# Performance work log

Measured on AMD Instinct MI355X. Metric: run time of the kernel, lower is better.

Reference implementation:

```python
import jax, jax.numpy as jnp
import numpy as np

N_EMBD = 512
N_HEAD = 8
D_HEAD = N_EMBD // N_HEAD
N_EXPERTS = 4
TOP_K = 2
D_FF = 4 * N_EMBD
EPS_RMS = 1e-5


def setup_inputs() -> dict:
    key = jax.random.key(0)
    ks = jax.random.split(key, 10)
    B, T, C = 8, 1024, N_EMBD
    s = 0.02
    return {
        "x": jax.random.normal(ks[0], (B, T, C), jnp.float32),
        "ln1_w": jnp.ones((C,), jnp.float32),
        "ln2_w": jnp.ones((C,), jnp.float32),
        "wq": jax.random.normal(ks[1], (C, C), jnp.float32) * s,
        "wk": jax.random.normal(ks[2], (C, C), jnp.float32) * s,
        "wv": jax.random.normal(ks[3], (C, C), jnp.float32) * s,
        "wo": jax.random.normal(ks[4], (C, C), jnp.float32) * s,
        "gate_w": jax.random.normal(ks[5], (N_EXPERTS, C), jnp.float32) * s,
        "w_fc": jax.random.normal(ks[6], (N_EXPERTS, D_FF, C), jnp.float32) * s,
        "w_proj": jax.random.normal(ks[7], (N_EXPERTS, C, D_FF), jnp.float32) * s,
    }


def rms_norm(x, w):
    var = jnp.mean(x * x, axis=-1, keepdims=True)
    return x * jax.lax.rsqrt(var + EPS_RMS) * w


def causal_attention(x, wq, wk, wv, wo):
    B, T, C = x.shape
    q = (x @ wq.T).reshape(B, T, N_HEAD, D_HEAD)
    k = (x @ wk.T).reshape(B, T, N_HEAD, D_HEAD)
    v = (x @ wv.T).reshape(B, T, N_HEAD, D_HEAD)
    scores = jnp.einsum("bqhd,bkhd->bhqk", q, k) / jnp.sqrt(jnp.float32(D_HEAD))
    mask = jnp.tril(jnp.ones((T, T), bool))
    scores = jnp.where(mask, scores, jnp.finfo(scores.dtype).min)
    attn = jax.nn.softmax(scores, axis=-1)
    out = jnp.einsum("bhqk,bkhd->bqhd", attn, v).reshape(B, T, C)
    return out @ wo.T


def ds_moe(x, gate_w, w_fc, w_proj):
    B, T, C = x.shape
    xf = x.reshape(B * T, C)                                # [N, C]
    gate_logits = xf @ gate_w.T                             # [N, E]
    gate_probs = jax.nn.softmax(gate_logits, axis=-1)
    topw, topi = jax.lax.top_k(gate_probs, TOP_K)           # [N, K]
    topw = topw / jnp.clip(topw.sum(-1, keepdims=True), 1e-6)
    # sparse router weights [N, E] (scatter of normalized top-k)
    sparse_w = jnp.zeros((xf.shape[0], N_EXPERTS), xf.dtype)
    sparse_w = sparse_w.at[jnp.arange(xf.shape[0])[:, None], topi].set(topw)
    # dense-equivalent expert compute: out = sum_e w_e * MLP_e(x)
    h = jax.nn.gelu(jnp.einsum("nc,efc->enf", xf, w_fc), approximate=False)
    eo = jnp.einsum("enf,ecf->enc", h, w_proj)              # [E, N, C]
    out = jnp.einsum("ne,enc->nc", sparse_w, eo)
    return out.reshape(B, T, C), sparse_w


def reference(x, ln1_w, ln2_w, wq, wk, wv, wo, gate_w, w_fc, w_proj):
    x = x + causal_attention(rms_norm(x, ln1_w), wq, wk, wv, wo)
    moe_out, router_w = ds_moe(rms_norm(x, ln2_w), gate_w, w_fc, w_proj)
    x = x + moe_out
    return x, router_w
```

## Files before the change

kernel.cpp:

```cpp
#include <hip/hip_runtime.h>
#include <math.h>

typedef __bf16 bf16_t;
typedef float    f32x2 __attribute__((ext_vector_type(2)));
typedef float    f32x4 __attribute__((ext_vector_type(4)));
typedef unsigned u32x2 __attribute__((ext_vector_type(2)));
typedef unsigned u32x4 __attribute__((ext_vector_type(4)));
typedef __bf16   bf16x8 __attribute__((ext_vector_type(8)));

#define WS_MB (size_t)(1u << 20)

__device__ __forceinline__ void gl16(const bf16_t* g, bf16_t* l) {
    void* gnc = const_cast<void*>((const void*)g);
    __builtin_amdgcn_global_load_lds((__attribute__((address_space(1))) void*)gnc,
                                     (__attribute__((address_space(3))) void*)l,
                                     16, 0, 0);
}

__device__ __forceinline__ float dot4(f32x4 a, f32x4 b) {
    return a.x * b.x + a.y * b.y + a.z * b.z + a.w * b.w;
}

__device__ __forceinline__ int xcd_swz(int orig, int nwg) {
    int q = nwg >> 3, r = nwg & 7;
    int x = orig & 7, i = orig >> 3;
    int base = (x < r) ? x * (q + 1) : r * (q + 1) + (x - r) * q;
    return base + i;
}

__global__ __launch_bounds__(256) void cvt_all_kernel(
    const float* __restrict__ s0, const float* __restrict__ s1,
    const float* __restrict__ s2, const float* __restrict__ s3,
    const float* __restrict__ s4, const float* __restrict__ s5,
    bf16_t* __restrict__ d0, bf16_t* __restrict__ d1,
    bf16_t* __restrict__ d2, bf16_t* __restrict__ d3,
    bf16_t* __restrict__ d4, bf16_t* __restrict__ d5,
    int* __restrict__ cnt) {
    if (blockIdx.x == 0 && threadIdx.x < 4) cnt[threadIdx.x] = 0;
    int i = blockIdx.x * 256 + threadIdx.x;
    const float* s; bf16_t* d; int off;
    if (i < 262144) {
        int seg = i >> 16; off = i & 65535;
        s = seg == 0 ? s0 : seg == 1 ? s1 : seg == 2 ? s2 : s3;
        d = seg == 0 ? d0 : seg == 1 ? d1 : seg == 2 ? d2 : d3;
    } else if (i < 1310720) { s = s4; d = d4; off = i - 262144; }
    else                    { s = s5; d = d5; off = i - 1310720; }
    f32x4 v = ((const f32x4*)s)[off];
    union { bf16_t b[4]; u32x2 u; } p;
    p.b[0] = (bf16_t)v.x; p.b[1] = (bf16_t)v.y;
    p.b[2] = (bf16_t)v.z; p.b[3] = (bf16_t)v.w;
    ((u32x2*)d)[off] = p.u;
}

__global__ __launch_bounds__(256) void rmsnorm_kernel(const float* __restrict__ x,
                                                      const float* __restrict__ w,
                                                      bf16_t* __restrict__ out) {
    int row = blockIdx.x;
    const float* xr = x + (size_t)row * 512;
    int t = threadIdx.x;
    f32x2 v = *(const f32x2*)(xr + t * 2);
    float ss = v.x * v.x + v.y * v.y;
#pragma unroll
    for (int o = 32; o > 0; o >>= 1) ss += __shfl_down(ss, o);
    __shared__ float red[4];
    if ((t & 63) == 0) red[t >> 6] = ss;
    __syncthreads();
    float tot = (red[0] + red[1]) + (red[2] + red[3]);
    float sc = rsqrtf(tot * (1.0f / 512.0f) + 1e-5f);
    f32x2 wv = *(const f32x2*)(w + t * 2);
    union { bf16_t b[2]; unsigned u; } p;
    p.b[0] = (bf16_t)(v.x * sc * wv.x);
    p.b[1] = (bf16_t)(v.y * sc * wv.y);
    *(unsigned*)(out + (size_t)row * 512 + t * 2) = p.u;
}

__device__ inline float gelu_fast(float x) {
    float u = -1.5957691216f * x * fmaf(0.044715f * x, x, 1.0f);
    return x / (1.0f + __expf(u));
}

#define GEMM_COMPUTE(LA, LB)                                                          \
    _Pragma("unroll")                                                                 \
    for (int kk = 0; kk < 2; ++kk) {                                                  \
        bf16x8 af[4], bfr[4];                                                         \
        _Pragma("unroll")                                                             \
        for (int mi = 0; mi < 4; mi++)                                                \
            af[mi] = *(const bf16x8*)((LA) + (wr + mi * 16 + lrow) * 64               \
                                      + (((kk * 4 + sg) ^ lr3) * 8));                 \
        _Pragma("unroll")                                                             \
        for (int ni = 0; ni < 4; ni++)                                                \
            bfr[ni] = *(const bf16x8*)((LB) + (wc + ni * 16 + lrow) * 64              \
                                       + (((kk * 4 + sg) ^ lr3) * 8));                \
        _Pragma("unroll")                                                             \
        for (int mi = 0; mi < 4; mi++) {                                              \
            _Pragma("unroll")                                                         \
            for (int ni = 0; ni < 4; ni++) {                                          \
                acc[mi][ni] = __builtin_amdgcn_mfma_f32_16x16x32_bf16(                \
                    af[mi], bfr[ni], acc[mi][ni], 0, 0, 0);                           \
            }                                                                         \
        }                                                                             \
    }

template <int EPI>
__global__ __launch_bounds__(256) void gemm_kernel(const bf16_t* __restrict__ A,
                                                   const bf16_t* __restrict__ B,
                                                   void* __restrict__ C,
                                                   const float* __restrict__ aux,
                                                   int N, int K, int ncol) {
    const int id = xcd_swz(blockIdx.x, gridDim.x);
    const int row0 = (id / ncol) * 128;
    const int col0 = (id % ncol) * 128;
    __shared__ __align__(16) bf16_t lds_a[128 * 64];
    __shared__ __align__(16) bf16_t lds_b[128 * 64];
    const int t = threadIdx.x;
    const bf16_t* Ap = A + (size_t)row0 * K;
    const bf16_t* Bp = B + (size_t)col0 * K;
    const int lane = t & 63, wave = t >> 6;
    const int wr = (wave >> 1) * 64, wc = (wave & 1) * 64;
    const int lrow = lane & 15;
    const int sg = lane >> 4, lr3 = lane & 7;
    const int srow = lane >> 3;
    const int scolx = ((lane & 7) ^ (lane >> 3)) * 8;

    f32x4 acc[4][4];
    f32x4 zero = {0.f, 0.f, 0.f, 0.f};
#pragma unroll
    for (int i = 0; i < 4; i++)
#pragma unroll
        for (int j = 0; j < 4; j++) acc[i][j] = zero;

    for (int k0 = 0; k0 < K; k0 += 64) {
        __syncthreads();
#pragma unroll
        for (int c = 0; c < 4; ++c) {
            const int rbase = wave * 32 + c * 8;
            gl16(Ap + (size_t)(rbase + srow) * K + k0 + scolx, lds_a + rbase * 64);
            gl16(Bp + (size_t)(rbase + srow) * K + k0 + scolx, lds_b + rbase * 64);
        }
        __syncthreads();
        GEMM_COMPUTE(lds_a, lds_b)
    }

#pragma unroll
    for (int mi = 0; mi < 4; mi++) {
        int rbase = row0 + wr + mi * 16 + (lane >> 4) * 4;
#pragma unroll
        for (int ni = 0; ni < 4; ni++) {
            int col = col0 + wc + ni * 16 + (lane & 15);
#pragma unroll
            for (int r = 0; r < 4; r++) {
                float v = acc[mi][ni][r];
                size_t idx = (size_t)(rbase + r) * N + col;
                if (EPI == 1) ((float*)C)[idx] = v + aux[idx];
                else          ((bf16_t*)C)[idx] = (bf16_t)v;
            }
        }
    }
}

__global__ __launch_bounds__(256) void moe_fc_kernel(
    const bf16_t* __restrict__ A, const bf16_t* __restrict__ B, bf16_t* __restrict__ H,
    const int* __restrict__ list, const int* __restrict__ cnt, const int* __restrict__ seg) {
    const int id = xcd_swz(blockIdx.x, gridDim.x);
    const int row0g = (id >> 5) * 128;
    const int col0 = (id & 31) * 64;
    int e = 0;
    if (row0g >= seg[1]) e = 1;
    if (row0g >= seg[2]) e = 2;
    if (row0g >= seg[3]) e = 3;
    const int ce = cnt[e];
    const int rl0 = row0g - seg[e];
    if (rl0 >= ce) return;

    __shared__ __align__(16) bf16_t lds_a[128 * 64];
    __shared__ __align__(16) bf16_t lds_b[64 * 64];
    const int t = threadIdx.x;
    const bf16_t* Bp = B + ((size_t)e * 2048 + col0) * 512;
    const int* le = list + e * 8192;
    const int lane = t & 63, wave = t >> 6;
    const int wr = (wave >> 1) * 64, wc = (wave & 1) * 32;
    const int lrow = lane & 15;
    const int sg = lane >> 4, lr3 = lane & 7;
    const int srow = lane >> 3;
    const int scolx = ((lane & 7) ^ (lane >> 3)) * 8;

    const bf16_t* Asrc[4];
#pragma unroll
    for (int c = 0; c < 4; ++c) {
        int r = rl0 + wave * 32 + c * 8 + srow;
        r = (r < ce) ? r : (ce - 1);
        Asrc[c] = A + (size_t)le[r] * 512 + scolx;
    }

    f32x4 acc[4][2];
    f32x4 zero = {0.f, 0.f, 0.f, 0.f};
#pragma unroll
    for (int i = 0; i < 4; i++)
#pragma unroll
        for (int j = 0; j < 2; j++) acc[i][j] = zero;

    for (int k0 = 0; k0 < 512; k0 += 64) {
        __syncthreads();
#pragma unroll
        for (int c = 0; c < 4; ++c) {
            const int rbase = wave * 32 + c * 8;
            gl16(Asrc[c] + k0, lds_a + rbase * 64);
        }
        {
            const int rbase = wave * 16;
            gl16(Bp + (size_t)(rbase + srow) * 512 + k0 + scolx, lds_b + rbase * 64);
            gl16(Bp + (size_t)(rbase + 8 + srow) * 512 + k0 + scolx, lds_b + (rbase + 8) * 64);
        }
        __syncthreads();
#pragma unroll
        for (int kk = 0; kk < 2; ++kk) {
            bf16x8 af[4], bfr[2];
#pragma unroll
            for (int mi = 0; mi < 4; mi++)
                af[mi] = *(const bf16x8*)(lds_a + (wr + mi * 16 + lrow) * 64
                                          + (((kk * 4 + sg) ^ lr3) * 8));
#pragma unroll
            for (int ni = 0; ni < 2; ni++)
                bfr[ni] = *(const bf16x8*)(lds_b + (wc + ni * 16 + lrow) * 64
                                           + (((kk * 4 + sg) ^ lr3) * 8));
#pragma unroll
            for (int mi = 0; mi < 4; mi++) {
#pragma unroll
                for (int ni = 0; ni < 2; ni++) {
                    acc[mi][ni] = __builtin_amdgcn_mfma_f32_16x16x32_bf16(
                        af[mi], bfr[ni], acc[mi][ni], 0, 0, 0);
                }
            }
        }
    }

#pragma unroll
    for (int mi = 0; mi < 4; mi++) {
        int rbase = row0g + wr + mi * 16 + (lane >> 4) * 4;
#pragma unroll
        for (int ni = 0; ni < 2; ni++) {
            int col = col0 + wc + ni * 16 + (lane & 15);
#pragma unroll
            for (int r = 0; r < 4; r++) {
                H[(size_t)(rbase + r) * 2048 + col] = (bf16_t)gelu_fast(acc[mi][ni][r]);
            }
        }
    }
}

__global__ __launch_bounds__(256) void moe_pj_kernel(
    const bf16_t* __restrict__ H, const bf16_t* __restrict__ B, float* __restrict__ xout,
    const float* __restrict__ rw, const int* __restrict__ list,
    const int* __restrict__ cnt, const int* __restrict__ seg) {
    const int id = xcd_swz(blockIdx.x, gridDim.x);
    const int row0g = (id >> 3) * 64;
    const int col0 = (id & 7) * 64;
    int e = 0;
    if (row0g >= seg[1]) e = 1;
    if (row0g >= seg[2]) e = 2;
    if (row0g >= seg[3]) e = 3;
    const int ce = cnt[e];
    const int se = seg[e];
    const int rl0 = row0g - se;
    if (rl0 >= ce) return;

    __shared__ __align__(16) bf16_t lds_a[64 * 64];
    __shared__ __align__(16) bf16_t lds_b[64 * 64];
    const int t = threadIdx.x;
    const bf16_t* Ap = H + (size_t)row0g * 2048;
    const bf16_t* Bp = B + ((size_t)e * 512 + col0) * 2048;
    const int* le = list + e * 8192;
    const int lane = t & 63, wave = t >> 6;
    const int wr = (wave >> 1) * 32, wc = (wave & 1) * 32;
    const int lrow = lane & 15;
    const int sg = lane >> 4, lr3 = lane & 7;
    const int srow = lane >> 3;
    const int scolx = ((lane & 7) ^ (lane >> 3)) * 8;

    f32x4 acc[2][2];
    f32x4 zero = {0.f, 0.f, 0.f, 0.f};
#pragma unroll
    for (int i = 0; i < 2; i++)
#pragma unroll
        for (int j = 0; j < 2; j++) acc[i][j] = zero;

    for (int k0 = 0; k0 < 2048; k0 += 64) {
        __syncthreads();
#pragma unroll
        for (int c = 0; c < 2; ++c) {
            const int rbase = wave * 16 + c * 8;
            gl16(Ap + (size_t)(rbase + srow) * 2048 + k0 + scolx, lds_a + rbase * 64);
            gl16(Bp + (size_t)(rbase + srow) * 2048 + k0 + scolx, lds_b + rbase * 64);
        }
        __syncthreads();
#pragma unroll
        for (int kk = 0; kk < 2; ++kk) {
            bf16x8 af[2], bfr[2];
#pragma unroll
            for (int mi = 0; mi < 2; mi++)
                af[mi] = *(const bf16x8*)(lds_a + (wr + mi * 16 + lrow) * 64
                                          + (((kk * 4 + sg) ^ lr3) * 8));
#pragma unroll
            for (int ni = 0; ni < 2; ni++)
                bfr[ni] = *(const bf16x8*)(lds_b + (wc + ni * 16 + lrow) * 64
                                           + (((kk * 4 + sg) ^ lr3) * 8));
#pragma unroll
            for (int mi = 0; mi < 2; mi++) {
#pragma unroll
                for (int ni = 0; ni < 2; ni++) {
                    acc[mi][ni] = __builtin_amdgcn_mfma_f32_16x16x32_bf16(
                        af[mi], bfr[ni], acc[mi][ni], 0, 0, 0);
                }
            }
        }
    }

#pragma unroll
    for (int mi = 0; mi < 2; mi++) {
        int rbase = row0g + wr + mi * 16 + (lane >> 4) * 4;
#pragma unroll
        for (int ni = 0; ni < 2; ni++) {
            int col = col0 + wc + ni * 16 + (lane & 15);
#pragma unroll
            for (int r = 0; r < 4; r++) {
                int rloc = rbase + r - se;
                if (rloc < ce) {
                    int tok = le[rloc];
                    atomicAdd(xout + (size_t)tok * 512 + col,
                              rw[(size_t)tok * 4 + e] * acc[mi][ni][r]);
                }
            }
        }
    }
}

__global__ __launch_bounds__(256) void attn_kernel(const bf16_t* __restrict__ QKV,
                                                   bf16_t* __restrict__ O) {
    __shared__ __align__(16) bf16_t klds[2 * 64 * 32];
    __shared__ __align__(16) bf16_t vlds[4 * 2 * 16 * 32];

    const int bx = blockIdx.x;
    const int qb = 15 - (bx >> 6);
    const int bh = bx & 63;
    const int b = bh >> 3, h = bh & 7;
    const int t = threadIdx.x;
    const int lane = t & 63, wave = t >> 6;
    const int g = lane >> 4, q15 = lane & 15;
    const int qbase = qb * 64 + wave * 16;
    const int qabs = qbase + q15;

    const bf16_t* Qb = QKV + (size_t)b * 1024 * 1536 + h * 64;
    const bf16_t* Kb = Qb + 512;
    const bf16_t* Vb = Qb + 1024;

    const bf16_t* qp = Qb + (size_t)qabs * 1536 + g * 8;
    bf16x8 qf0 = *(const bf16x8*)(qp);
    bf16x8 qf1 = *(const bf16x8*)(qp + 32);

    f32x4 acc[4];
    f32x4 zero = {0.f, 0.f, 0.f, 0.f};
#pragma unroll
    for (int i = 0; i < 4; i++) acc[i] = zero;
    float m = -1e30f, denom = 0.f;

    const int kr1 = t >> 3, kc1 = t & 7;
    const int vr = t & 63, vc1 = t >> 6, vc2 = vc1 + 4;
    const int perm = ((q15 >> 2) * 8) + (q15 & 3);

    const int nkt = qb + 1;
    u32x4 ka  = *(const u32x4*)(Kb + (size_t)(kr1) * 1536 + kc1 * 8);
    u32x4 kb2 = *(const u32x4*)(Kb + (size_t)(kr1 + 32) * 1536 + kc1 * 8);
    u32x4 va  = *(const u32x4*)(Vb + (size_t)(vr) * 1536 + vc1 * 8);
    u32x4 vb2 = *(const u32x4*)(Vb + (size_t)(vr) * 1536 + vc2 * 8);

    for (int kt = 0; kt < nkt; ++kt) {
        __syncthreads();
        *(u32x4*)(klds + (kc1 >> 2) * 2048 + kr1 * 32 + (kc1 & 3) * 8) = ka;
        *(u32x4*)(klds + (kc1 >> 2) * 2048 + (kr1 + 32) * 32 + (kc1 & 3) * 8) = kb2;
        {
            union { u32x4 u; bf16_t e[8]; } tv;
            const int kh = vr >> 5, k32 = vr & 31;
            tv.u = va;
#pragma unroll
            for (int j = 0; j < 8; ++j) {
                int d = vc1 * 8 + j;
                vlds[(((d >> 4) * 2 + kh) * 16 + (d & 15)) * 32 + k32] = tv.e[j];
            }
            tv.u = vb2;
#pragma unroll
            for (int j = 0; j < 8; ++j) {
                int d = vc2 * 8 + j;
                vlds[(((d >> 4) * 2 + kh) * 16 + (d & 15)) * 32 + k32] = tv.e[j];
            }
        }
        __syncthreads();

        if (kt + 1 < nkt) {
            const size_t krow = (size_t)((kt + 1) * 64);
            ka  = *(const u32x4*)(Kb + (krow + kr1) * 1536 + kc1 * 8);
            kb2 = *(const u32x4*)(Kb + (krow + kr1 + 32) * 1536 + kc1 * 8);
            va  = *(const u32x4*)(Vb + (krow + vr) * 1536 + vc1 * 8);
            vb2 = *(const u32x4*)(Vb + (krow + vr) * 1536 + vc2 * 8);
        }

        for (int s32 = 0; s32 < 2; ++s32) {
            const int KB = kt * 64 + s32 * 32;
            if (KB > qbase + 15) break;
            const int r0 = s32 * 32 + perm;
            bf16x8 k00 = *(const bf16x8*)(klds + r0 * 32 + g * 8);
            bf16x8 k01 = *(const bf16x8*)(klds + 2048 + r0 * 32 + g * 8);
            bf16x8 k10 = *(const bf16x8*)(klds + (r0 + 4) * 32 + g * 8);
            bf16x8 k11 = *(const bf16x8*)(klds + 2048 + (r0 + 4) * 32 + g * 8);
            f32x4 s0 = zero, s1 = zero;
            s0 = __builtin_amdgcn_mfma_f32_16x16x32_bf16(k00, qf0, s0, 0, 0, 0);
            s0 = __builtin_amdgcn_mfma_f32_16x16x32_bf16(k01, qf1, s0, 0, 0, 0);
            s1 = __builtin_amdgcn_mfma_f32_16x16x32_bf16(k10, qf0, s1, 0, 0, 0);
            s1 = __builtin_amdgcn_mfma_f32_16x16x32_bf16(k11, qf1, s1, 0, 0, 0);

            const int kbg = KB + 8 * g;
            float sv[8];
#pragma unroll
            for (int r = 0; r < 4; ++r) {
                sv[r]     = (kbg + r     <= qabs) ? s0[r] * 0.125f : -1e30f;
                sv[4 + r] = (kbg + 4 + r <= qabs) ? s1[r] * 0.125f : -1e30f;
            }
            float tm = sv[0];
#pragma unroll
            for (int j = 1; j < 8; ++j) tm = fmaxf(tm, sv[j]);
            tm = fmaxf(tm, __shfl_xor(tm, 16));
            tm = fmaxf(tm, __shfl_xor(tm, 32));
            const float mn = fmaxf(m, tm);
            const float co = __expf(m - mn);
            float p[8];
            float ts = 0.f;
#pragma unroll
            for (int j = 0; j < 8; ++j) { p[j] = __expf(sv[j] - mn); ts += p[j]; }
            ts += __shfl_xor(ts, 16);
            ts += __shfl_xor(ts, 32);
            denom = denom * co + ts;
            m = mn;
            union { bf16_t e[8]; bf16x8 v; } pp;
#pragma unroll
            for (int j = 0; j < 8; ++j) pp.e[j] = (bf16_t)p[j];

#pragma unroll
            for (int db = 0; db < 4; ++db) {
                acc[db] *= co;
                bf16x8 vf = *(const bf16x8*)(vlds + ((db * 2 + s32) * 16 + q15) * 32 + g * 8);
                acc[db] = __builtin_amdgcn_mfma_f32_16x16x32_bf16(vf, pp.v, acc[db], 0, 0, 0);
            }
        }
    }

    const float inv = 1.0f / denom;
    bf16_t* op = O + (size_t)b * 1024 * 512 + h * 64 + (size_t)qabs * 512;
#pragma unroll
    for (int db = 0; db < 4; ++db) {
        union { bf16_t e[4]; u32x2 u; } w;
#pragma unroll
        for (int r = 0; r < 4; ++r) w.e[r] = (bf16_t)(acc[db][r] * inv);
        *(u32x2*)(op + db * 16 + g * 4) = w.u;
    }
}

__global__ void seg_kernel(const int* __restrict__ cnt, int* __restrict__ seg) {
    if (threadIdx.x == 0) {
        int b = 0;
#pragma unroll
        for (int e = 0; e < 4; ++e) { seg[e] = b; b += (cnt[e] + 127) & ~127; }
    }
}

__global__ __launch_bounds__(256) void router_kernel(
    const float* __restrict__ xr, const float* __restrict__ w,
    const float* __restrict__ gw, bf16_t* __restrict__ hb,
    float* __restrict__ rout, int* __restrict__ list, int* __restrict__ cnt) {
    __shared__ int lcnt[4], gb[4];
    __shared__ int ent_tok[64], ent_e[64], ent_r[64];
    const int t = threadIdx.x, lane = t & 63, wave = t >> 6;
    if (t < 4) lcnt[t] = 0;
    __syncthreads();

    const f32x4 w0  = *(const f32x4*)(w + lane * 8);
    const f32x4 w1  = *(const f32x4*)(w + lane * 8 + 4);
    const f32x4 g00 = *(const f32x4*)(gw + lane * 8);
    const f32x4 g01 = *(const f32x4*)(gw + lane * 8 + 4);
    const f32x4 g10 = *(const f32x4*)(gw + 512 + lane * 8);
    const f32x4 g11 = *(const f32x4*)(gw + 512 + lane * 8 + 4);
    const f32x4 g20 = *(const f32x4*)(gw + 1024 + lane * 8);
    const f32x4 g21 = *(const f32x4*)(gw + 1024 + lane * 8 + 4);
    const f32x4 g30 = *(const f32x4*)(gw + 1536 + lane * 8);
    const f32x4 g31 = *(const f32x4*)(gw + 1536 + lane * 8 + 4);

    for (int it = 0; it < 8; ++it) {
        const int tok = blockIdx.x * 32 + wave * 8 + it;
        const float* row = xr + (size_t)tok * 512 + lane * 8;
        f32x4 v0 = *(const f32x4*)(row);
        f32x4 v1 = *(const f32x4*)(row + 4);
        float ss = dot4(v0, v0) + dot4(v1, v1);
        f32x4 xw0, xw1;
        xw0.x = v0.x * w0.x; xw0.y = v0.y * w0.y; xw0.z = v0.z * w0.z; xw0.w = v0.w * w0.w;
        xw1.x = v1.x * w1.x; xw1.y = v1.y * w1.y; xw1.z = v1.z * w1.z; xw1.w = v1.w * w1.w;
        float d0 = dot4(xw0, g00) + dot4(xw1, g01);
        float d1 = dot4(xw0, g10) + dot4(xw1, g11);
        float d2 = dot4(xw0, g20) + dot4(xw1, g21);
        float d3 = dot4(xw0, g30) + dot4(xw1, g31);
#pragma unroll
        for (int o = 32; o > 0; o >>= 1) {
            ss += __shfl_xor(ss, o);
            d0 += __shfl_xor(d0, o);
            d1 += __shfl_xor(d1, o);
            d2 += __shfl_xor(d2, o);
            d3 += __shfl_xor(d3, o);
        }
        const float sc = rsqrtf(ss * (1.0f / 512.0f) + 1e-5f);
        union { bf16_t b[8]; u32x4 u; } hw;
        hw.b[0] = (bf16_t)(xw0.x * sc); hw.b[1] = (bf16_t)(xw0.y * sc);
        hw.b[2] = (bf16_t)(xw0.z * sc); hw.b[3] = (bf16_t)(xw0.w * sc);
        hw.b[4] = (bf16_t)(xw1.x * sc); hw.b[5] = (bf16_t)(xw1.y * sc);
        hw.b[6] = (bf16_t)(xw1.z * sc); hw.b[7] = (bf16_t)(xw1.w * sc);
        *(u32x4*)(hb + (size_t)tok * 512 + lane * 8) = hw.u;

        const float l0 = d0 * sc, l1 = d1 * sc, l2 = d2 * sc, l3 = d3 * sc;
        float mx = fmaxf(fmaxf(l0, l1), fmaxf(l2, l3));
        float p[4];
        p[0] = expf(l0 - mx); p[1] = expf(l1 - mx);
        p[2] = expf(l2 - mx); p[3] = expf(l3 - mx);
        float s = (p[0] + p[1]) + (p[2] + p[3]);
        float is = 1.0f / s;
        p[0] *= is; p[1] *= is; p[2] *= is; p[3] *= is;
        int i0 = 0; float b0 = p[0];
#pragma unroll
        for (int e = 1; e < 4; e++) if (p[e] > b0) { b0 = p[e]; i0 = e; }
        int i1 = -1; float b1 = -1.f;
#pragma unroll
        for (int e = 0; e < 4; e++) {
            if (e == i0) continue;
            if (p[e] > b1) { b1 = p[e]; i1 = e; }
        }
        if (lane == 0) {
            float inv2 = 1.0f / fmaxf(b0 + b1, 1e-6f);
            float o[4] = {0.f, 0.f, 0.f, 0.f};
            o[i0] = b0 * inv2;
            o[i1] = b1 * inv2;
            f32x4 ov; ov.x = o[0]; ov.y = o[1]; ov.z = o[2]; ov.w = o[3];
            *(f32x4*)(rout + (size_t)tok * 4) = ov;
            int r0 = atomicAdd(&lcnt[i0], 1);
            int r1 = atomicAdd(&lcnt[i1], 1);
            int ei = (wave * 8 + it) * 2;
            ent_tok[ei] = tok;     ent_e[ei] = i0;     ent_r[ei] = r0;
            ent_tok[ei + 1] = tok; ent_e[ei + 1] = i1; ent_r[ei + 1] = r1;
        }
    }
    __syncthreads();
    if (t < 4) gb[t] = atomicAdd(&cnt[t], lcnt[t]);
    __syncthreads();
    if (t < 64) {
        int e = ent_e[t];
        list[e * 8192 + gb[e] + ent_r[t]] = ent_tok[t];
    }
}

extern "C" void kernel_launch(void* const* d_in, const int* in_sizes, int n_in,
                              void* d_out, int out_size, void* d_ws, size_t ws_size,
                              hipStream_t stream) {
    (void)in_sizes; (void)n_in; (void)out_size; (void)ws_size;
    const float* x   = (const float*)d_in[0];
    const float* ln1 = (const float*)d_in[1];
    const float* ln2 = (const float*)d_in[2];
    const float* wq  = (const float*)d_in[3];
    const float* wk  = (const float*)d_in[4];
    const float* wv  = (const float*)d_in[5];
    const float* wo  = (const float*)d_in[6];
    const float* gw  = (const float*)d_in[7];
    const float* wfc = (const float*)d_in[8];
    const float* wpj = (const float*)d_in[9];

    char* ws = (char*)d_ws;
    bf16_t* hb    = (bf16_t*)(ws);
    bf16_t* qkvb  = (bf16_t*)(ws + 8 * WS_MB);
    bf16_t* attb  = (bf16_t*)(ws + 32 * WS_MB);
    bf16_t* Hb    = (bf16_t*)(ws + 8 * WS_MB);
    bf16_t* wqkvb = (bf16_t*)(ws + 74 * WS_MB);
    bf16_t* wob   = (bf16_t*)(ws + 74 * WS_MB + 1536 * 1024);
    bf16_t* wfcb  = (bf16_t*)(ws + 76 * WS_MB);
    bf16_t* wpjb  = (bf16_t*)(ws + 84 * WS_MB);
    int*    list  = (int*)(ws + 92 * WS_MB);
    int*    cnt   = (int*)(ws + 92 * WS_MB + 192 * 1024);
    int*    seg   = cnt + 8;

    float* xout   = (float*)d_out;
    float* router = xout + (size_t)8192 * 512;

    cvt_all_kernel<<<9216, 256, 0, stream>>>(wq, wk, wv, wo, wfc, wpj,
                                             wqkvb, wqkvb + 512 * 512, wqkvb + 1024 * 512,
                                             wob, wfcb, wpjb, cnt);

    rmsnorm_kernel<<<8192, 256, 0, stream>>>(x, ln1, hb);
    gemm_kernel<4><<<768, 256, 0, stream>>>(hb, wqkvb, (void*)qkvb, nullptr, 1536, 512, 12);

    attn_kernel<<<1024, 256, 0, stream>>>(qkvb, attb);

    gemm_kernel<1><<<256, 256, 0, stream>>>(attb, wob, (void*)xout, x, 512, 512, 4);

    router_kernel<<<256, 256, 0, stream>>>(xout, ln2, gw, hb, router, list, cnt);
    seg_kernel<<<1, 64, 0, stream>>>(cnt, seg);

    moe_fc_kernel<<<32 * 131, 256, 0, stream>>>(hb, wfcb, Hb, list, cnt, seg);
    moe_pj_kernel<<<8 * 262, 256, 0, stream>>>(Hb, wpjb, xout, router, list, cnt, seg);
}
```

Baseline: 229.8 us.

## Widen cvt and rmsnorm to 8 elements per thread, add setprio around attention MFMAs

The weight conversion kernel now converts 8 floats per thread with 16-byte stores, using half as many blocks. RMSNorm processes one row per wave with shuffle-only reduction and 8 elements per lane, dropping the shared-memory barrier and launching a quarter as many blocks. In attention, s_setprio raises wave priority around the MFMA groups to favour matrix issue over the softmax work of other waves. These target memory efficiency and launch/barrier overhead in small kernels, at the cost of fewer waves per kernel.

```diff
diff --git a/kernel.cpp b/kernel.cpp
--- a/kernel.cpp
+++ b/kernel.cpp
@@ -39,39 +39,42 @@
     if (blockIdx.x == 0 && threadIdx.x < 4) cnt[threadIdx.x] = 0;
     int i = blockIdx.x * 256 + threadIdx.x;
     const float* s; bf16_t* d; int off;
-    if (i < 262144) {
-        int seg = i >> 16; off = i & 65535;
-        s = seg == 0 ? s0 : seg == 1 ? s1 : seg == 2 ? s2 : s3;
-        d = seg == 0 ? d0 : seg == 1 ? d1 : seg == 2 ? d2 : d3;
-    } else if (i < 1310720) { s = s4; d = d4; off = i - 262144; }
-    else                    { s = s5; d = d5; off = i - 1310720; }
-    f32x4 v = ((const f32x4*)s)[off];
-    union { bf16_t b[4]; u32x2 u; } p;
-    p.b[0] = (bf16_t)v.x; p.b[1] = (bf16_t)v.y;
-    p.b[2] = (bf16_t)v.z; p.b[3] = (bf16_t)v.w;
-    ((u32x2*)d)[off] = p.u;
+    if (i < 131072) {
+        int sg8 = i >> 15; off = i & 32767;
+        s = sg8 == 0 ? s0 : sg8 == 1 ? s1 : sg8 == 2 ? s2 : s3;
+        d = sg8 == 0 ? d0 : sg8 == 1 ? d1 : sg8 == 2 ? d2 : d3;
+    } else if (i < 655360) { s = s4; d = d4; off = i - 131072; }
+    else                   { s = s5; d = d5; off = i - 655360; }
+    f32x4 v0 = ((const f32x4*)s)[off * 2];
+    f32x4 v1 = ((const f32x4*)s)[off * 2 + 1];
+    union { bf16_t b[8]; u32x4 u; } p;
+    p.b[0] = (bf16_t)v0.x; p.b[1] = (bf16_t)v0.y;
+    p.b[2] = (bf16_t)v0.z; p.b[3] = (bf16_t)v0.w;
+    p.b[4] = (bf16_t)v1.x; p.b[5] = (bf16_t)v1.y;
+    p.b[6] = (bf16_t)v1.z; p.b[7] = (bf16_t)v1.w;
+    ((u32x4*)d)[off] = p.u;
 }
 
 __global__ __launch_bounds__(256) void rmsnorm_kernel(const float* __restrict__ x,
                                                       const float* __restrict__ w,
                                                       bf16_t* __restrict__ out) {
-    int row = blockIdx.x;
-    const float* xr = x + (size_t)row * 512;
-    int t = threadIdx.x;
-    f32x2 v = *(const f32x2*)(xr + t * 2);
-    float ss = v.x * v.x + v.y * v.y;
-#pragma unroll
-    for (int o = 32; o > 0; o >>= 1) ss += __shfl_down(ss, o);
-    __shared__ float red[4];
-    if ((t & 63) == 0) red[t >> 6] = ss;
-    __syncthreads();
-    float tot = (red[0] + red[1]) + (red[2] + red[3]);
-    float sc = rsqrtf(tot * (1.0f / 512.0f) + 1e-5f);
-    f32x2 wv = *(const f32x2*)(w + t * 2);
-    union { bf16_t b[2]; unsigned u; } p;
-    p.b[0] = (bf16_t)(v.x * sc * wv.x);
-    p.b[1] = (bf16_t)(v.y * sc * wv.y);
-    *(unsigned*)(out + (size_t)row * 512 + t * 2) = p.u;
+    const int t = threadIdx.x, lane = t & 63, wave = t >> 6;
+    const int row = blockIdx.x * 4 + wave;
+    const float* xr = x + (size_t)row * 512 + lane * 8;
+    f32x4 v0 = *(const f32x4*)(xr);
+    f32x4 v1 = *(const f32x4*)(xr + 4);
+    float ss = dot4(v0, v0) + dot4(v1, v1);
+#pragma unroll
+    for (int o = 32; o > 0; o >>= 1) ss += __shfl_xor(ss, o);
+    float sc = rsqrtf(ss * (1.0f / 512.0f) + 1e-5f);
+    f32x4 w0 = *(const f32x4*)(w + lane * 8);
+    f32x4 w1 = *(const f32x4*)(w + lane * 8 + 4);
+    union { bf16_t b[8]; u32x4 u; } p;
+    p.b[0] = (bf16_t)(v0.x * sc * w0.x); p.b[1] = (bf16_t)(v0.y * sc * w0.y);
+    p.b[2] = (bf16_t)(v0.z * sc * w0.z); p.b[3] = (bf16_t)(v0.w * sc * w0.w);
+    p.b[4] = (bf16_t)(v1.x * sc * w1.x); p.b[5] = (bf16_t)(v1.y * sc * w1.y);
+    p.b[6] = (bf16_t)(v1.z * sc * w1.z); p.b[7] = (bf16_t)(v1.w * sc * w1.w);
+    *(u32x4*)(out + (size_t)row * 512 + lane * 8) = p.u;
 }
 
 __device__ inline float gelu_fast(float x) {
@@ -412,10 +415,12 @@
             bf16x8 k10 = *(const bf16x8*)(klds + (r0 + 4) * 32 + g * 8);
             bf16x8 k11 = *(const bf16x8*)(klds + 2048 + (r0 + 4) * 32 + g * 8);
             f32x4 s0 = zero, s1 = zero;
+            __builtin_amdgcn_s_setprio(1);
             s0 = __builtin_amdgcn_mfma_f32_16x16x32_bf16(k00, qf0, s0, 0, 0, 0);
             s0 = __builtin_amdgcn_mfma_f32_16x16x32_bf16(k01, qf1, s0, 0, 0, 0);
             s1 = __builtin_amdgcn_mfma_f32_16x16x32_bf16(k10, qf0, s1, 0, 0, 0);
             s1 = __builtin_amdgcn_mfma_f32_16x16x32_bf16(k11, qf1, s1, 0, 0, 0);
+            __builtin_amdgcn_s_setprio(0);
 
             const int kbg = KB + 8 * g;
             float sv[8];
@@ -443,12 +448,14 @@
 #pragma unroll
             for (int j = 0; j < 8; ++j) pp.e[j] = (bf16_t)p[j];
 
+            __builtin_amdgcn_s_setprio(1);
 #pragma unroll
             for (int db = 0; db < 4; ++db) {
                 acc[db] *= co;
                 bf16x8 vf = *(const bf16x8*)(vlds + ((db * 2 + s32) * 16 + q15) * 32 + g * 8);
                 acc[db] = __builtin_amdgcn_mfma_f32_16x16x32_bf16(vf, pp.v, acc[db], 0, 0, 0);
             }
+            __builtin_amdgcn_s_setprio(0);
         }
     }
 
@@ -592,11 +599,11 @@
     float* xout   = (float*)d_out;
     float* router = xout + (size_t)8192 * 512;
 
-    cvt_all_kernel<<<9216, 256, 0, stream>>>(wq, wk, wv, wo, wfc, wpj,
+    cvt_all_kernel<<<4608, 256, 0, stream>>>(wq, wk, wv, wo, wfc, wpj,
                                              wqkvb, wqkvb + 512 * 512, wqkvb + 1024 * 512,
                                              wob, wfcb, wpjb, cnt);
 
-    rmsnorm_kernel<<<8192, 256, 0, stream>>>(x, ln1, hb);
+    rmsnorm_kernel<<<2048, 256, 0, stream>>>(x, ln1, hb);
     gemm_kernel<4><<<768, 256, 0, stream>>>(hb, wqkvb, (void*)qkvb, nullptr, 1536, 512, 12);
 
     attn_kernel<<<1024, 256, 0, stream>>>(qkvb, attb);
```

After: 226.5 us. Within noise of the previous version (-1.5%).
